# Kernel optimization log

Hardware: AMD Instinct MI355X
Metric: run time of the kernel (lower is better)

Reference implementation:

```python
import jax, jax.numpy as jnp
import numpy as np

HS = 64      # head_size
MS = 2048    # memory_size
NH = 4       # num_heads
H = 512      # hidden_size


def setup_inputs() -> dict:
    key = jax.random.key(0)
    ks = jax.random.split(key, 6)
    B, T, I, O = 32, 32, 256, 256
    ctrl_in = I + NH * HS  # 512

    def p(k, shape, fan):
        return jax.random.normal(k, shape, jnp.float32) / np.sqrt(fan).astype(np.float32)

    return {
        "x": jax.random.normal(ks[0], (B, T, I), jnp.float32),
        "W_ih": p(ks[1], (4 * H, ctrl_in), ctrl_in),
        "W_hh": p(ks[2], (4 * H, H), H),
        "b_ih": jnp.zeros((4 * H,), jnp.float32),
        "b_hh": jnp.zeros((4 * H,), jnp.float32),
        "W_head": p(ks[3], (NH * (HS + MS + 3), H), H),
        "b_head": jnp.zeros((NH * (HS + MS + 3),), jnp.float32),
        "W_out": p(ks[4], (O, H + NH * HS), H + NH * HS),
        "b_out": jnp.zeros((O,), jnp.float32),
    }


def reference(x, W_ih, W_hh, b_ih, b_hh, W_head, b_head, W_out, b_out):
    B, T, _ = x.shape
    scale = 1.0 / np.sqrt(HS).astype(np.float32)

    def step(carry, x_t):
        h, c, mem, read = carry
        # controller LSTM cell (PyTorch gate order i,f,g,o)
        inp = jnp.concatenate([x_t, read.reshape(B, -1)], axis=-1)
        gates = inp @ W_ih.T + b_ih + h @ W_hh.T + b_hh
        i, f, g, o = jnp.split(gates, 4, axis=-1)
        c = jax.nn.sigmoid(f) * c + jax.nn.sigmoid(i) * jnp.tanh(g)
        h = jax.nn.sigmoid(o) * jnp.tanh(c)
        # head params: [B, NH, HS + MS + 3]
        hp = (h @ W_head.T + b_head).reshape(B, NH, HS + MS + 3)
        # read addressing (uses memory BEFORE write)
        read_keys = hp[:, :, :HS]
        rw = jax.nn.softmax(jnp.einsum('bnk,bmk->bnm', read_keys, mem) * scale, axis=-1)
        read = jnp.einsum('bnm,bmh->bnh', rw, mem)
        # write addressing
        write_keys = hp[:, :, HS:2 * HS]
        write_strength = jax.nn.sigmoid(hp[:, :, 2 * HS:2 * HS + 1])
        ww = jax.nn.softmax(jnp.einsum('bnk,bmk->bnm', write_keys, mem) * scale, axis=-1)
        mem = mem + jnp.einsum('bnm,bnh->bmh', ww, write_strength * write_keys)
        # output projection
        out = jnp.concatenate([h, read.reshape(B, -1)], axis=-1) @ W_out.T + b_out
        return (h, c, mem, read), out

    h0 = jnp.zeros((B, H), x.dtype)
    c0 = jnp.zeros((B, H), x.dtype)
    mem0 = jnp.zeros((B, MS, HS), x.dtype)
    read0 = jnp.zeros((B, NH, HS), x.dtype)
    (h, c, mem, _), outs = jax.lax.scan(step, (h0, c0, mem0, read0), jnp.swapaxes(x, 0, 1))
    outputs = jnp.swapaxes(outs, 0, 1)  # [B, T, O]
    return outputs, mem, (h, c)
```

## Files before the change

### kernel.cpp

```cpp
#include <hip/hip_runtime.h>
#include <math.h>

#define B 32
#define T 32
#define O_DIM 256
#define H_DIM 512
#define HS 64
#define MS 2048
#define NCOL 516
#define NCH 32

typedef __attribute__((ext_vector_type(4))) float f4;

__device__ __forceinline__ float sigm(float x){ return 1.0f/(1.0f+__expf(-x)); }
__device__ __forceinline__ float hsum(f4 v){ return (v.x + v.y) + (v.z + v.w); }

__global__ __launch_bounds__(256) void k_transpose_t(float* __restrict__ dst,
                                                     const float* __restrict__ src,
                                                     int N, int K){
  __shared__ float tile[32][33];
  int jb = blockIdx.x*32, kb = blockIdx.y*32;
  int tj = threadIdx.x & 31, tk = threadIdx.x >> 5;
  #pragma unroll
  for (int p = 0; p < 4; ++p){
    int j = jb + tk + p*8, k = kb + tj;
    if (j < N && k < K) tile[tk + p*8][tj] = src[j*K + k];
  }
  __syncthreads();
  #pragma unroll
  for (int p = 0; p < 4; ++p){
    int k = kb + tk + p*8, j = jb + tj;
    if (j < N && k < K) dst[k*N + j] = tile[tj][tk + p*8];
  }
}

__global__ __launch_bounds__(256) void k_ghead(float* __restrict__ dst,
                                               const float* __restrict__ W_head){
  int idx = blockIdx.x*256 + threadIdx.x;
  if (idx >= 520*512) return;
  int col = idx >> 9, k = idx & 511;
  float v = 0.f;
  if (col < NCOL){ int n = col/129, c = col%129; v = W_head[((size_t)n*2115 + c)*512 + k]; }
  dst[idx] = v;
}

__global__ __launch_bounds__(256) void k_xt(f4* __restrict__ XT4,
                                            const float* __restrict__ x){
  int idx = blockIdx.x*256 + threadIdx.x;
  int b = idx & 31, k4 = (idx >> 5) & 63, t = idx >> 11;
  XT4[idx] = ((const f4*)x)[(size_t)(b*T + t)*64 + k4];
}

__global__ __launch_bounds__(512) void k_A(
    const f4* __restrict__ XT4, const float* __restrict__ W_ih,
    const float* __restrict__ W_hh, const float* __restrict__ b_ih,
    const float* __restrict__ b_hh, const f4* __restrict__ READT4,
    float* __restrict__ HHT, float* __restrict__ CF, int t)
{
  __shared__ f4 WS[8*256];
  __shared__ float glp[2][8][33];
  const int bid = blockIdx.x, tid = threadIdx.x;
  const f4* HHT4 = (const f4*)HHT;
  for (int idx = tid; idx < 2048; idx += 512){
    int rsub = idx >> 8, q = idx & 255;
    int gate = rsub & 3, jj = (rsub >> 2) & 1;
    int row = gate*512 + bid*2 + jj;
    WS[idx] = (q < 128) ? ((const f4*)W_ih)[(size_t)row*128 + q]
                        : ((const f4*)W_hh)[(size_t)row*128 + (q - 128)];
  }
  __syncthreads();
  {
    int b = tid & 31, rsub = (tid >> 5) & 7, khalf = tid >> 8;
    const f4* w = WS + rsub*256;
    f4 a0 = {0.f,0.f,0.f,0.f}, a1 = {0.f,0.f,0.f,0.f};
    if (khalf == 0){
      const f4* xt4 = XT4 + (size_t)t*2048;
      #pragma unroll 4
      for (int k4 = 0; k4 < 64; k4 += 2){
        a0 += w[k4]     * xt4[k4*32 + b];
        a1 += w[k4+1]   * xt4[(k4+1)*32 + b];
      }
      #pragma unroll 4
      for (int k4 = 0; k4 < 64; k4 += 2){
        a0 += w[64+k4]   * READT4[k4*32 + b];
        a1 += w[64+k4+1] * READT4[(k4+1)*32 + b];
      }
    } else if (t > 0){
      const f4* ht4 = HHT4 + (size_t)(t-1)*4096;
      #pragma unroll 4
      for (int k4 = 0; k4 < 128; k4 += 2){
        a0 += w[128+k4]   * ht4[k4*32 + b];
        a1 += w[128+k4+1] * ht4[(k4+1)*32 + b];
      }
    }
    glp[khalf][rsub][b] = hsum(a0 + a1);
  }
  __syncthreads();
  if (tid < 64){
    int b2 = tid & 31, jj2 = tid >> 5;
    int j2 = bid*2 + jj2;
    int r0 = 0*512 + j2, r1 = 1*512 + j2, r2 = 2*512 + j2, r3 = 3*512 + j2;
    float gi = glp[0][jj2*4+0][b2] + glp[1][jj2*4+0][b2] + b_ih[r0] + b_hh[r0];
    float gf = glp[0][jj2*4+1][b2] + glp[1][jj2*4+1][b2] + b_ih[r1] + b_hh[r1];
    float gg = glp[0][jj2*4+2][b2] + glp[1][jj2*4+2][b2] + b_ih[r2] + b_hh[r2];
    float go = glp[0][jj2*4+3][b2] + glp[1][jj2*4+3][b2] + b_ih[r3] + b_hh[r3];
    float c = sigm(gf)*CF[b2*512+j2] + sigm(gi)*tanhf(gg);
    float h = sigm(go)*tanhf(c);
    CF[b2*512+j2] = c;
    HHT[((size_t)t*128 + (j2>>2))*128 + b2*4 + (j2&3)] = h;
  }
}

__global__ __launch_bounds__(256) void k_B(
    const float* __restrict__ HHT, const float* __restrict__ WT_HD2,
    const float* __restrict__ b_head, float* __restrict__ HPT, int t)
{
  __shared__ float red[256];
  const int bid = blockIdx.x, tid = threadIdx.x;
  const f4* HHT4 = (const f4*)HHT;
  int b = tid & 31, cs = (tid>>5)&1, kq = tid>>6;
  int col = bid*2 + cs;
  const f4* hT4 = HHT4 + (size_t)t*4096 + kq*1024;
  const f4* w4  = (const f4*)(WT_HD2 + (size_t)col*512) + kq*32;
  f4 acc4 = {0.f, 0.f, 0.f, 0.f};
  #pragma unroll 4
  for (int k4 = 0; k4 < 32; ++k4)
    acc4 += w4[k4] * hT4[k4*32 + b];
  red[tid] = hsum(acc4);
  __syncthreads();
  if (kq == 0){
    float v = red[tid] + red[tid + 64] + red[tid + 128] + red[tid + 192];
    if (col < NCOL){ int n = col/129, c = col%129; v += b_head[n*2115 + c]; }
    HPT[col*32 + b] = v;
  }
}

__global__ __launch_bounds__(512) void k_CD(
    float* __restrict__ MEM, const float* __restrict__ HPT,
    float* __restrict__ SW, float* __restrict__ PART, float* __restrict__ PREAD,
    const float* __restrict__ WST, const float* __restrict__ WKS, int t)
{
  __shared__ float keys[8][64];
  __shared__ float mc[2][64][68];
  __shared__ float sc[2][4][64];
  __shared__ float ew[2][4][64];
  __shared__ f4 wkp[4][16];
  __shared__ float gmp[4], facp[4];
  const int bid = blockIdx.x, tid = threadIdx.x;
  f4* MEM4 = (f4*)MEM;
  int xcd = bid & 7, t2 = bid >> 3;
  int b = xcd*4 + (t2 & 3), ch8 = t2 >> 2;
  int hkh = tid >> 8, tl = tid & 255;
  if (tid < 512){
    int kk = tid >> 6, e = tid & 63;
    int n = kk & 3;
    int c = (kk >= 4) ? (64 + e) : e;
    keys[kk][e] = HPT[(n*129 + c)*32 + b];
  }
  if (t > 0){
    if (tid < 64){
      int n = tid >> 4, e4 = tid & 15;
      wkp[n][e4] = ((const f4*)WKS)[(b*4 + n)*16 + e4];
    }
    if (tid < 4){ gmp[tid] = WST[b*8 + tid*2]; facp[tid] = WST[b*8 + tid*2 + 1]; }
  }
  for (int sub = 0; sub < 2; ++sub){
    int ch = ch8*4 + hkh*2 + sub;
    __syncthreads();
    for (int idx = tl; idx < 64*16; idx += 256){
      int m = idx >> 4, e4 = idx & 15;
      ((f4*)&mc[hkh][m][0])[e4] = MEM4[((size_t)b*MS + ch*64 + m)*16 + e4];
    }
    if (t > 0){
      int n = tl >> 6, m = tl & 63;
      float s = SW[((size_t)b*4 + n)*MS + ch*64 + m];
      ew[hkh][n][m] = __expf(s - gmp[n]) * facp[n];
    }
    __syncthreads();
    if (t > 0){
      for (int idx = tl; idx < 1024; idx += 256){
        int m = idx >> 4, e4 = idx & 15;
        f4 v = ((f4*)&mc[hkh][m][0])[e4];
        v += ew[hkh][0][m]*wkp[0][e4] + ew[hkh][1][m]*wkp[1][e4]
           + ew[hkh][2][m]*wkp[2][e4] + ew[hkh][3][m]*wkp[3][e4];
        ((f4*)&mc[hkh][m][0])[e4] = v;
        MEM4[((size_t)b*MS + ch*64 + m)*16 + e4] = v;
      }
      __syncthreads();
    }
    {
      int m = tl & 63, kp = tl >> 6;
      const f4* mrow4 = (const f4*)&mc[hkh][m][0];
      int k0 = kp*2, k1 = kp*2+1;
      f4 s0v = {0.f,0.f,0.f,0.f}, s1v = {0.f,0.f,0.f,0.f};
      #pragma unroll 4
      for (int e4 = 0; e4 < 16; ++e4){
        f4 mv = mrow4[e4];
        s0v += mv * (*(const f4*)&keys[k0][e4*4]);
        s1v += mv * (*(const f4*)&keys[k1][e4*4]);
      }
      float s0 = hsum(s0v)*0.125f, s1 = hsum(s1v)*0.125f;
      if (kp >= 2){
        float* swp = SW + ((size_t)b*4 + (k0-4))*MS + ch*64 + m;
        swp[0] = s0; swp[MS] = s1;
      }
      float mx0 = s0, mx1 = s1;
      #pragma unroll
      for (int off = 32; off > 0; off >>= 1){
        mx0 = fmaxf(mx0, __shfl_xor(mx0, off, 64));
        mx1 = fmaxf(mx1, __shfl_xor(mx1, off, 64));
      }
      float e0 = __expf(s0 - mx0), e1 = __expf(s1 - mx1);
      float sm0 = e0, sm1 = e1;
      #pragma unroll
      for (int off = 32; off > 0; off >>= 1){
        sm0 += __shfl_xor(sm0, off, 64);
        sm1 += __shfl_xor(sm1, off, 64);
      }
      if (kp < 2){ sc[hkh][k0][m] = e0; sc[hkh][k1][m] = e1; }
      if (m == 0){
        float* pp = PART + (((size_t)b*NCH + ch)*8 + k0)*2;
        pp[0] = mx0; pp[1] = sm0;
        pp[2] = mx1; pp[3] = sm1;
      }
    }
    __syncthreads();
    {
      int n = tl >> 6, e = tl & 63;
      float pr = 0.f;
      for (int m = 0; m < 64; ++m) pr += sc[hkh][n][m] * mc[hkh][m][e];
      PREAD[(((size_t)b*NCH + ch)*4 + n)*64 + e] = pr;
    }
  }
}

__global__ __launch_bounds__(256) void k_Dlite(
    const float* __restrict__ HPT, const float* __restrict__ PART,
    const float* __restrict__ PREAD, float* __restrict__ READT,
    float* __restrict__ RHIST, float* __restrict__ WST, float* __restrict__ WKS,
    const float* __restrict__ HHT, float* __restrict__ HF, int t)
{
  __shared__ float dn2[4];
  __shared__ float ef[4][32];
  const int bid = blockIdx.x, tid = threadIdx.x;
  const f4* HHT4 = (const f4*)HHT;
  int b = (bid & 7)*4 + (bid >> 3);
  {
    int kk = tid >> 5, ch = tid & 31;
    const float* pp = PART + (((size_t)b*NCH + ch)*8 + kk)*2;
    float m0 = pp[0], s0 = pp[1];
    float mx = m0;
    #pragma unroll
    for (int off = 16; off > 0; off >>= 1)
      mx = fmaxf(mx, __shfl_xor(mx, off, 32));
    float d = s0 * __expf(m0 - mx);
    #pragma unroll
    for (int off = 16; off > 0; off >>= 1)
      d += __shfl_xor(d, off, 32);
    if (kk < 4){
      ef[kk][ch] = __expf(m0 - mx);
      if (ch == 0) dn2[kk] = d;
    } else if (ch == 0){
      float st = sigm(HPT[((kk-4)*129 + 128)*32 + b]);
      WST[b*8 + (kk-4)*2]     = mx;
      WST[b*8 + (kk-4)*2 + 1] = st / d;
    }
  }
  {
    int n = tid >> 6, e = tid & 63;
    WKS[(b*4 + n)*64 + e] = HPT[(n*129 + 64 + e)*32 + b];
  }
  __syncthreads();
  {
    int n = tid >> 6, e = tid & 63;
    const float* prp = PREAD + ((size_t)b*NCH*4 + n)*64 + e;
    float r = 0.f;
    #pragma unroll 8
    for (int ch = 0; ch < NCH; ++ch)
      r += prp[(size_t)ch*256] * ef[n][ch];
    r /= dn2[n];
    int k = n*64 + e;
    READT[(k>>2)*128 + b*4 + (k&3)] = r;
    RHIST[((size_t)t*64 + (k>>2))*128 + b*4 + (k&3)] = r;
  }
  if (t == T-1){
    int i = bid*256 + tid;
    if (i < 4096){
      int j4 = i & 127, bb = i >> 7;
      ((f4*)HF)[i] = HHT4[((size_t)(T-1)*128 + j4)*32 + bb];
    }
  }
}

__global__ __launch_bounds__(256) void k_flush(
    float* __restrict__ MEM, const float* __restrict__ SW,
    const float* __restrict__ WST, const float* __restrict__ WKS)
{
  __shared__ float gm[4], fac[4];
  __shared__ f4 wk4[4][16];
  __shared__ float ew[4][256];
  const int bid = blockIdx.x, tid = threadIdx.x;
  int xcd = bid & 7, t2 = bid >> 3;
  int b = xcd*4 + (t2 & 3), sub = t2 >> 2;
  if (tid < 4){ gm[tid] = WST[b*8 + tid*2]; fac[tid] = WST[b*8 + tid*2 + 1]; }
  if (tid < 64){
    int n = tid >> 4, e4 = tid & 15;
    wk4[n][e4] = ((const f4*)WKS)[(b*4 + n)*16 + e4];
  }
  __syncthreads();
  for (int idx = tid; idx < 1024; idx += 256){
    int n = idx >> 8, m = idx & 255;
    float s = SW[((size_t)b*4 + n)*MS + sub*256 + m];
    ew[n][m] = __expf(s - gm[n]) * fac[n];
  }
  __syncthreads();
  {
    int e4 = tid & 15, ms = tid >> 4;
    f4 k0 = wk4[0][e4], k1 = wk4[1][e4], k2 = wk4[2][e4], k3 = wk4[3][e4];
    #pragma unroll 2
    for (int it = 0; it < 16; ++it){
      int m = it*16 + ms;
      float w0 = ew[0][m], w1 = ew[1][m];
      float w2 = ew[2][m], w3 = ew[3][m];
      f4* p = (f4*)MEM + ((size_t)b*MS + sub*256 + m)*16 + e4;
      f4 v = *p;
      v += w0*k0 + w1*k1 + w2*k2 + w3*k3;
      *p = v;
    }
  }
}

__global__ __launch_bounds__(256) void k_out(
    const float* __restrict__ HHT, const float* __restrict__ RHIST,
    const float* __restrict__ WT_OUT, const float* __restrict__ b_out,
    float* __restrict__ out)
{
  __shared__ float A[16][260];
  const int bid = blockIdx.x, tid = threadIdx.x;
  const f4* HHT4 = (const f4*)HHT;
  const f4* RHIST4 = (const f4*)RHIST;
  const f4* W4 = (const f4*)WT_OUT;
  int nt = bid & 3, mt = bid >> 2;
  int rl = tid & 15, og = tid >> 4;
  int o = nt*64 + og*4, o4 = o >> 2;
  f4 a0 = {0.f,0.f,0.f,0.f}, a1 = a0, a2 = a0, a3 = a0;
  for (int kc = 0; kc < 3; ++kc){
    __syncthreads();
    for (int idx = tid; idx < 1024; idx += 256){
      int r = idx >> 6, k4 = idx & 63;
      int row = mt*16 + r;
      int bb = row >> 5, tt = row & 31;
      int kg4 = kc*64 + k4;
      f4 v = (kg4 < 128)
        ? HHT4[((size_t)tt*128 + kg4)*32 + bb]
        : RHIST4[((size_t)tt*64 + (kg4-128))*32 + bb];
      *(f4*)&A[r][k4*4] = v;
    }
    __syncthreads();
    const float* Ar = &A[rl][0];
    const f4* wp = W4 + (size_t)kc*256*64 + o4;
    #pragma unroll 2
    for (int k = 0; k < 256; k += 4){
      a0 += Ar[k]   * wp[(size_t)(k)*64];
      a1 += Ar[k+1] * wp[(size_t)(k+1)*64];
      a2 += Ar[k+2] * wp[(size_t)(k+2)*64];
      a3 += Ar[k+3] * wp[(size_t)(k+3)*64];
    }
  }
  int row = mt*16 + rl;
  f4 accv = (a0 + a1) + (a2 + a3);
  accv += *(const f4*)(b_out + o);
  *(f4*)(out + (size_t)row*O_DIM + o) = accv;
}

extern "C" void kernel_launch(void* const* d_in, const int* in_sizes, int n_in,
                              void* d_out, int out_size, void* d_ws, size_t ws_size,
                              hipStream_t stream)
{
  const float* x      = (const float*)d_in[0];
  const float* W_ih   = (const float*)d_in[1];
  const float* W_hh   = (const float*)d_in[2];
  const float* b_ih   = (const float*)d_in[3];
  const float* b_hh   = (const float*)d_in[4];
  const float* W_head = (const float*)d_in[5];
  const float* b_head = (const float*)d_in[6];
  const float* W_out  = (const float*)d_in[7];
  const float* b_out  = (const float*)d_in[8];

  float* out = (float*)d_out;
  float* MEM = out + B*T*O_DIM;
  float* HF  = MEM + (size_t)B*MS*HS;
  float* CF  = HF + B*H_DIM;

  float* ws      = (float*)d_ws;
  float* WT_HD2  = ws;
  float* WT_OUT  = WT_HD2 + 520*512;
  float* XT      = WT_OUT + 768*256;
  float* SW      = XT     + 262144;
  float* PART    = SW     + 262144;
  float* PREAD   = PART   + 16384;
  float* HPT     = PREAD  + 262144;
  float* READT   = HPT    + 16640;
  float* HHT     = READT  + 8192;
  float* RHIST   = HHT    + 524288;
  float* WST     = RHIST  + 262144;
  float* WKS     = WST    + 256;

  (void)hipMemsetAsync(MEM, 0, ((size_t)B*MS*HS + 2*B*H_DIM)*sizeof(float), stream);
  (void)hipMemsetAsync(READT, 0, (size_t)8192*sizeof(float), stream);

  k_ghead<<<1040, 256, 0, stream>>>(WT_HD2, W_head);
  k_transpose_t<<<dim3(8, 24), 256, 0, stream>>>(WT_OUT, W_out, 256, 768);
  k_xt<<<256, 256, 0, stream>>>((f4*)XT, x);

  for (int t = 0; t < T; ++t){
    k_A<<<256, 512, 0, stream>>>((const f4*)XT, W_ih, W_hh, b_ih, b_hh,
                                 (const f4*)READT, HHT, CF, t);
    k_B<<<260, 256, 0, stream>>>(HHT, WT_HD2, b_head, HPT, t);
    k_CD<<<256, 512, 0, stream>>>(MEM, HPT, SW, PART, PREAD, WST, WKS, t);
    k_Dlite<<<32, 256, 0, stream>>>(HPT, PART, PREAD, READT, RHIST, WST, WKS,
                                    HHT, HF, t);
  }
  k_flush<<<256, 256, 0, stream>>>(MEM, SW, WST, WKS);
  k_out<<<256, 256, 0, stream>>>(HHT, RHIST, WT_OUT, b_out, out);
}
```

Baseline: 1.185 ms.

## Move deferred memory write-update into LSTM kernel as extra blocks

The previous step's memory write update (exp of saved scores times write keys added into MEM) moves out of k_CD and into 256 extra blocks appended to the LSTM gate kernel. The update then runs alongside the LSTM matvec instead of on k_CD's critical path, so k_CD only reads memory. The cost is that MEM is written by one kernel and re-read by k_CD, rather than updated in shared memory and reused in place, which adds global memory traffic.

```diff
diff --git a/kernel.cpp b/kernel.cpp
--- a/kernel.cpp
+++ b/kernel.cpp
@@ -51,63 +51,102 @@
   XT4[idx] = ((const f4*)x)[(size_t)(b*T + t)*64 + k4];
 }
 
-__global__ __launch_bounds__(512) void k_A(
+__global__ __launch_bounds__(512) void k_AU(
     const f4* __restrict__ XT4, const float* __restrict__ W_ih,
     const float* __restrict__ W_hh, const float* __restrict__ b_ih,
     const float* __restrict__ b_hh, const f4* __restrict__ READT4,
-    float* __restrict__ HHT, float* __restrict__ CF, int t)
+    float* __restrict__ HHT, float* __restrict__ CF,
+    float* __restrict__ MEM, const float* __restrict__ SW,
+    const float* __restrict__ WST, const float* __restrict__ WKS, int t)
 {
   __shared__ f4 WS[8*256];
   __shared__ float glp[2][8][33];
+  __shared__ float gm[4], fac[4];
+  __shared__ f4 wk4[4][16];
+  __shared__ float ew[4][256];
   const int bid = blockIdx.x, tid = threadIdx.x;
   const f4* HHT4 = (const f4*)HHT;
-  for (int idx = tid; idx < 2048; idx += 512){
-    int rsub = idx >> 8, q = idx & 255;
-    int gate = rsub & 3, jj = (rsub >> 2) & 1;
-    int row = gate*512 + bid*2 + jj;
-    WS[idx] = (q < 128) ? ((const f4*)W_ih)[(size_t)row*128 + q]
-                        : ((const f4*)W_hh)[(size_t)row*128 + (q - 128)];
-  }
-  __syncthreads();
-  {
-    int b = tid & 31, rsub = (tid >> 5) & 7, khalf = tid >> 8;
-    const f4* w = WS + rsub*256;
-    f4 a0 = {0.f,0.f,0.f,0.f}, a1 = {0.f,0.f,0.f,0.f};
-    if (khalf == 0){
-      const f4* xt4 = XT4 + (size_t)t*2048;
-      #pragma unroll 4
-      for (int k4 = 0; k4 < 64; k4 += 2){
-        a0 += w[k4]     * xt4[k4*32 + b];
-        a1 += w[k4+1]   * xt4[(k4+1)*32 + b];
-      }
-      #pragma unroll 4
-      for (int k4 = 0; k4 < 64; k4 += 2){
-        a0 += w[64+k4]   * READT4[k4*32 + b];
-        a1 += w[64+k4+1] * READT4[(k4+1)*32 + b];
-      }
-    } else if (t > 0){
-      const f4* ht4 = HHT4 + (size_t)(t-1)*4096;
-      #pragma unroll 4
-      for (int k4 = 0; k4 < 128; k4 += 2){
-        a0 += w[128+k4]   * ht4[k4*32 + b];
-        a1 += w[128+k4+1] * ht4[(k4+1)*32 + b];
-      }
-    }
-    glp[khalf][rsub][b] = hsum(a0 + a1);
-  }
-  __syncthreads();
-  if (tid < 64){
-    int b2 = tid & 31, jj2 = tid >> 5;
-    int j2 = bid*2 + jj2;
-    int r0 = 0*512 + j2, r1 = 1*512 + j2, r2 = 2*512 + j2, r3 = 3*512 + j2;
-    float gi = glp[0][jj2*4+0][b2] + glp[1][jj2*4+0][b2] + b_ih[r0] + b_hh[r0];
-    float gf = glp[0][jj2*4+1][b2] + glp[1][jj2*4+1][b2] + b_ih[r1] + b_hh[r1];
-    float gg = glp[0][jj2*4+2][b2] + glp[1][jj2*4+2][b2] + b_ih[r2] + b_hh[r2];
-    float go = glp[0][jj2*4+3][b2] + glp[1][jj2*4+3][b2] + b_ih[r3] + b_hh[r3];
-    float c = sigm(gf)*CF[b2*512+j2] + sigm(gi)*tanhf(gg);
-    float h = sigm(go)*tanhf(c);
-    CF[b2*512+j2] = c;
-    HHT[((size_t)t*128 + (j2>>2))*128 + b2*4 + (j2&3)] = h;
+
+  if (bid < 256){
+    for (int idx = tid; idx < 2048; idx += 512){
+      int rsub = idx >> 8, q = idx & 255;
+      int gate = rsub & 3, jj = (rsub >> 2) & 1;
+      int row = gate*512 + bid*2 + jj;
+      WS[idx] = (q < 128) ? ((const f4*)W_ih)[(size_t)row*128 + q]
+                          : ((const f4*)W_hh)[(size_t)row*128 + (q - 128)];
+    }
+    __syncthreads();
+    {
+      int b = tid & 31, rsub = (tid >> 5) & 7, khalf = tid >> 8;
+      const f4* w = WS + rsub*256;
+      f4 a0 = {0.f,0.f,0.f,0.f}, a1 = {0.f,0.f,0.f,0.f};
+      if (khalf == 0){
+        const f4* xt4 = XT4 + (size_t)t*2048;
+        #pragma unroll 4
+        for (int k4 = 0; k4 < 64; k4 += 2){
+          a0 += w[k4]     * xt4[k4*32 + b];
+          a1 += w[k4+1]   * xt4[(k4+1)*32 + b];
+        }
+        #pragma unroll 4
+        for (int k4 = 0; k4 < 64; k4 += 2){
+          a0 += w[64+k4]   * READT4[k4*32 + b];
+          a1 += w[64+k4+1] * READT4[(k4+1)*32 + b];
+        }
+      } else if (t > 0){
+        const f4* ht4 = HHT4 + (size_t)(t-1)*4096;
+        #pragma unroll 4
+        for (int k4 = 0; k4 < 128; k4 += 2){
+          a0 += w[128+k4]   * ht4[k4*32 + b];
+          a1 += w[128+k4+1] * ht4[(k4+1)*32 + b];
+        }
+      }
+      glp[khalf][rsub][b] = hsum(a0 + a1);
+    }
+    __syncthreads();
+    if (tid < 64){
+      int b2 = tid & 31, jj2 = tid >> 5;
+      int j2 = bid*2 + jj2;
+      int r0 = 0*512 + j2, r1 = 1*512 + j2, r2 = 2*512 + j2, r3 = 3*512 + j2;
+      float gi = glp[0][jj2*4+0][b2] + glp[1][jj2*4+0][b2] + b_ih[r0] + b_hh[r0];
+      float gf = glp[0][jj2*4+1][b2] + glp[1][jj2*4+1][b2] + b_ih[r1] + b_hh[r1];
+      float gg = glp[0][jj2*4+2][b2] + glp[1][jj2*4+2][b2] + b_ih[r2] + b_hh[r2];
+      float go = glp[0][jj2*4+3][b2] + glp[1][jj2*4+3][b2] + b_ih[r3] + b_hh[r3];
+      float c = sigm(gf)*CF[b2*512+j2] + sigm(gi)*tanhf(gg);
+      float h = sigm(go)*tanhf(c);
+      CF[b2*512+j2] = c;
+      HHT[((size_t)t*128 + (j2>>2))*128 + b2*4 + (j2&3)] = h;
+    }
+  } else {
+    if (t == 0) return;
+    int i = bid - 256;
+    int xcd = i & 7, r2 = i >> 3;
+    int b = xcd*4 + (r2 & 3), sub = r2 >> 2;
+    if (tid < 4){ gm[tid] = WST[b*8 + tid*2]; fac[tid] = WST[b*8 + tid*2 + 1]; }
+    if (tid < 64){
+      int n = tid >> 4, e4 = tid & 15;
+      wk4[n][e4] = ((const f4*)WKS)[(b*4 + n)*16 + e4];
+    }
+    __syncthreads();
+    for (int idx = tid; idx < 1024; idx += 512){
+      int n = idx >> 8, m = idx & 255;
+      float s = SW[((size_t)b*4 + n)*MS + sub*256 + m];
+      ew[n][m] = __expf(s - gm[n]) * fac[n];
+    }
+    __syncthreads();
+    {
+      int e4 = tid & 15, ms = tid >> 4;
+      f4 k0 = wk4[0][e4], k1 = wk4[1][e4], k2 = wk4[2][e4], k3 = wk4[3][e4];
+      #pragma unroll 2
+      for (int it = 0; it < 8; ++it){
+        int m = it*32 + ms;
+        float w0 = ew[0][m], w1 = ew[1][m];
+        float w2 = ew[2][m], w3 = ew[3][m];
+        f4* p = (f4*)MEM + ((size_t)b*MS + sub*256 + m)*16 + e4;
+        f4 v = *p;
+        v += w0*k0 + w1*k1 + w2*k2 + w3*k3;
+        *p = v;
+      }
+    }
   }
 }
 
@@ -136,18 +175,15 @@
 }
 
 __global__ __launch_bounds__(512) void k_CD(
-    float* __restrict__ MEM, const float* __restrict__ HPT,
+    const float* __restrict__ MEM, const float* __restrict__ HPT,
     float* __restrict__ SW, float* __restrict__ PART, float* __restrict__ PREAD,
-    const float* __restrict__ WST, const float* __restrict__ WKS, int t)
+    int t)
 {
   __shared__ float keys[8][64];
   __shared__ float mc[2][64][68];
   __shared__ float sc[2][4][64];
-  __shared__ float ew[2][4][64];
-  __shared__ f4 wkp[4][16];
-  __shared__ float gmp[4], facp[4];
-  const int bid = blockIdx.x, tid = threadIdx.x;
-  f4* MEM4 = (f4*)MEM;
+  const int bid = blockIdx.x, tid = threadIdx.x;
+  const f4* MEM4 = (const f4*)MEM;
   int xcd = bid & 7, t2 = bid >> 3;
   int b = xcd*4 + (t2 & 3), ch8 = t2 >> 2;
   int hkh = tid >> 8, tl = tid & 255;
@@ -157,13 +193,6 @@
     int c = (kk >= 4) ? (64 + e) : e;
     keys[kk][e] = HPT[(n*129 + c)*32 + b];
   }
-  if (t > 0){
-    if (tid < 64){
-      int n = tid >> 4, e4 = tid & 15;
-      wkp[n][e4] = ((const f4*)WKS)[(b*4 + n)*16 + e4];
-    }
-    if (tid < 4){ gmp[tid] = WST[b*8 + tid*2]; facp[tid] = WST[b*8 + tid*2 + 1]; }
-  }
   for (int sub = 0; sub < 2; ++sub){
     int ch = ch8*4 + hkh*2 + sub;
     __syncthreads();
@@ -171,23 +200,7 @@
       int m = idx >> 4, e4 = idx & 15;
       ((f4*)&mc[hkh][m][0])[e4] = MEM4[((size_t)b*MS + ch*64 + m)*16 + e4];
     }
-    if (t > 0){
-      int n = tl >> 6, m = tl & 63;
-      float s = SW[((size_t)b*4 + n)*MS + ch*64 + m];
-      ew[hkh][n][m] = __expf(s - gmp[n]) * facp[n];
-    }
-    __syncthreads();
-    if (t > 0){
-      for (int idx = tl; idx < 1024; idx += 256){
-        int m = idx >> 4, e4 = idx & 15;
-        f4 v = ((f4*)&mc[hkh][m][0])[e4];
-        v += ew[hkh][0][m]*wkp[0][e4] + ew[hkh][1][m]*wkp[1][e4]
-           + ew[hkh][2][m]*wkp[2][e4] + ew[hkh][3][m]*wkp[3][e4];
-        ((f4*)&mc[hkh][m][0])[e4] = v;
-        MEM4[((size_t)b*MS + ch*64 + m)*16 + e4] = v;
-      }
-      __syncthreads();
-    }
+    __syncthreads();
     {
       int m = tl & 63, kp = tl >> 6;
       const f4* mrow4 = (const f4*)&mc[hkh][m][0];
@@ -414,10 +427,11 @@
   k_xt<<<256, 256, 0, stream>>>((f4*)XT, x);
 
   for (int t = 0; t < T; ++t){
-    k_A<<<256, 512, 0, stream>>>((const f4*)XT, W_ih, W_hh, b_ih, b_hh,
-                                 (const f4*)READT, HHT, CF, t);
+    k_AU<<<512, 512, 0, stream>>>((const f4*)XT, W_ih, W_hh, b_ih, b_hh,
+                                  (const f4*)READT, HHT, CF,
+                                  MEM, SW, WST, WKS, t);
     k_B<<<260, 256, 0, stream>>>(HHT, WT_HD2, b_head, HPT, t);
-    k_CD<<<256, 512, 0, stream>>>(MEM, HPT, SW, PART, PREAD, WST, WKS, t);
+    k_CD<<<256, 512, 0, stream>>>(MEM, HPT, SW, PART, PREAD, t);
     k_Dlite<<<32, 256, 0, stream>>>(HPT, PART, PREAD, READT, RHIST, WST, WKS,
                                     HHT, HF, t);
   }
```

Result: faster. 1.116 ms, median of 2 (-5.9%).
